# Kernel optimization log

Hardware: AMD Instinct MI355X
Metric: run time of the kernel (lower is better)

## Reference

```python
import jax, jax.numpy as jnp
import numpy as np

HEAD_DIM = 128
L2_EPS = 1e-6


def l2norm(x):
    # RMS-style L2Norm: computed in fp32, cast back (matches L2Norm.forward)
    x32 = x.astype(jnp.float32)
    y = x32 * jax.lax.rsqrt(jnp.mean(x32 * x32, axis=-1, keepdims=True) + L2_EPS)
    return y.astype(x.dtype)


def setup_inputs() -> dict:
    key = jax.random.key(0)
    ks = jax.random.split(key, 8)
    B, S, D = 16, 1, 4096
    NKV, HD, MAXS = 8, HEAD_DIM, 4096
    w_scale = 0.02
    return {
        "x": jax.random.normal(ks[0], (B, S, D), dtype=jnp.float32),
        "wq": jax.random.normal(ks[1], (D, D), dtype=jnp.float32) * w_scale,
        "wk": jax.random.normal(ks[2], (D, NKV * HD), dtype=jnp.float32) * w_scale,
        "wv": jax.random.normal(ks[3], (D, NKV * HD), dtype=jnp.float32) * w_scale,
        "wo": jax.random.normal(ks[4], (D, D), dtype=jnp.float32) * w_scale,
        "cache_k": jax.random.normal(ks[5], (B, MAXS, NKV, HD), dtype=jnp.float32),
        "cache_v": jax.random.normal(ks[6], (B, MAXS, NKV, HD), dtype=jnp.float32),
        "freqs_complex": jax.random.normal(ks[7], (1, 64), dtype=jnp.float32),  # unused, as in source
        "start_pos": 4095,
    }


def reference(x, wq, wk, wv, wo, cache_k, cache_v, freqs_complex, start_pos):
    b, s, d = x.shape
    hd = HEAD_DIM
    n_kv = cache_k.shape[2]
    n_q = wq.shape[1] // hd
    n_rep = n_q // n_kv

    # QKV projections (Linear, no bias)
    xq = (x @ wq).reshape(b, s, n_q, hd)
    xk = (x @ wk).reshape(b, s, n_kv, hd)
    xv = (x @ wv).reshape(b, s, n_kv, hd)

    # qk_norm active since dim <= 4096
    xq = l2norm(xq)
    xk = l2norm(xk)

    # KV-cache append at start_pos (start_pos is a static Python int)
    cache_k = jax.lax.dynamic_update_slice(cache_k, xk, (0, start_pos, 0, 0))
    cache_v = jax.lax.dynamic_update_slice(cache_v, xv, (0, start_pos, 0, 0))
    keys = cache_k[:, : start_pos + s]    # [b, T, n_kv, hd]
    values = cache_v[:, : start_pos + s]  # [b, T, n_kv, hd]

    # GQA: group query heads as (n_kv, n_rep); equivalent to repeat_kv without
    # materializing the repeated KV tensors.
    xq = xq.reshape(b, s, n_kv, n_rep, hd)
    scores = jnp.einsum("bqgrd,bkgd->bgrqk", xq, keys) / np.float32(np.sqrt(hd))
    scores = jax.nn.softmax(scores.astype(jnp.float32), axis=-1).astype(xq.dtype)
    out = jnp.einsum("bgrqk,bkgd->bqgrd", scores, values).reshape(b, s, n_q * hd)
    return out @ wo
```

## Files before the change

### kernel.cpp

```cpp
#include <hip/hip_runtime.h>

#define D_MODEL 4096
#define NKV     8
#define NREP    4
#define HD      128
#define BATCH   16
#define SEQ     4096
#define NCOLS   6144
#define SPLITS  32
#define KC      128
#define NS      8
#define CHUNK   512

#define OFF_QKVP 0
#define OFF_QKV  3145728
#define OFF_ATTO 3244032
#define OFF_ATTM 3768320
#define OFF_ATTL 3772416
#define OFF_XO   3776512

__global__ __launch_bounds__(256) void qkv_partial(
    const float* __restrict__ x, const float* __restrict__ wq,
    const float* __restrict__ wk, const float* __restrict__ wv,
    float* __restrict__ part)
{
  int tid = threadIdx.x;
  int col = blockIdx.x * 256 + tid;
  int sp  = blockIdx.y;
  const float* w; int c; int N;
  if (col < 4096)      { w = wq; c = col;        N = 4096; }
  else if (col < 5120) { w = wk; c = col - 4096; N = 1024; }
  else                 { w = wv; c = col - 5120; N = 1024; }
  int k0 = sp * KC;
  const float* wp = w + (size_t)k0 * N + c;
  float acc[BATCH];
#pragma unroll
  for (int b = 0; b < BATCH; ++b) acc[b] = 0.f;
  for (int kk = 0; kk < KC; kk += 4) {
    float w0 = wp[0];
    float w1 = wp[N];
    float w2 = wp[2 * N];
    float w3 = wp[3 * N];
#pragma unroll
    for (int b = 0; b < BATCH; ++b) {
      float4 xb = *reinterpret_cast<const float4*>(x + b * D_MODEL + k0 + kk);
      acc[b] = fmaf(xb.x, w0, fmaf(xb.y, w1, fmaf(xb.z, w2, fmaf(xb.w, w3, acc[b]))));
    }
    wp += (size_t)4 * N;
  }
#pragma unroll
  for (int b = 0; b < BATCH; ++b)
    part[(size_t)(sp * BATCH + b) * NCOLS + col] = acc[b];
}

__global__ __launch_bounds__(128) void qkv_finalize(
    const float* __restrict__ part, float* __restrict__ qkv)
{
  __shared__ float red[2];
  int blk = blockIdx.x;
  int b = blk / 48, h = blk - b * 48;
  int col = h * HD + threadIdx.x;
  float v = 0.f;
#pragma unroll
  for (int s = 0; s < SPLITS; ++s)
    v += part[(size_t)(s * BATCH + b) * NCOLS + col];
  float ss = v * v;
#pragma unroll
  for (int off = 32; off; off >>= 1) ss += __shfl_xor(ss, off);
  if ((threadIdx.x & 63) == 0) red[threadIdx.x >> 6] = ss;
  __syncthreads();
  float tot = red[0] + red[1];
  if (h < 40)
    v *= rsqrtf(tot * (1.f / 128.f) + 1e-6f);
  qkv[(size_t)b * NCOLS + col] = v;
}

__global__ __launch_bounds__(256) void attn_partial(
    const float* __restrict__ cache_k, const float* __restrict__ cache_v,
    const float* __restrict__ qkv,
    float* __restrict__ attO, float* __restrict__ attM, float* __restrict__ attL)
{
  __shared__ float qs[NREP * HD];
  __shared__ float sc[NREP * CHUNK];
  __shared__ float op[4 * NREP * HD];
  __shared__ float ml[8];
  int tid = threadIdx.x;
  int sp = blockIdx.x;
  int bg = blockIdx.y;
  int b = bg >> 3, g = bg & 7;

  const float* qsrc = qkv + (size_t)b * NCOLS + g * (NREP * HD);
  for (int i = tid; i < NREP * HD; i += 256) qs[i] = qsrc[i];
  __syncthreads();

  int pos0 = sp * CHUNK;
  const float* kbase = cache_k + ((size_t)b * SEQ * NKV + g) * HD;
#pragma unroll
  for (int t = 0; t < 2; ++t) {
    int pos = pos0 + t * 256 + tid;
    const float* kv = (pos == SEQ - 1)
        ? (qkv + (size_t)b * NCOLS + 4096 + g * HD)
        : (kbase + (size_t)pos * (NKV * HD));
    float a0 = 0.f, a1 = 0.f, a2 = 0.f, a3 = 0.f;
    for (int d = 0; d < HD; d += 4) {
      float4 kk = *reinterpret_cast<const float4*>(kv + d);
      float4 q0 = *reinterpret_cast<const float4*>(qs + 0 * HD + d);
      float4 q1 = *reinterpret_cast<const float4*>(qs + 1 * HD + d);
      float4 q2 = *reinterpret_cast<const float4*>(qs + 2 * HD + d);
      float4 q3 = *reinterpret_cast<const float4*>(qs + 3 * HD + d);
      a0 += kk.x*q0.x + kk.y*q0.y + kk.z*q0.z + kk.w*q0.w;
      a1 += kk.x*q1.x + kk.y*q1.y + kk.z*q1.z + kk.w*q1.w;
      a2 += kk.x*q2.x + kk.y*q2.y + kk.z*q2.z + kk.w*q2.w;
      a3 += kk.x*q3.x + kk.y*q3.y + kk.z*q3.z + kk.w*q3.w;
    }
    const float scl = 0.08838834764831845f;
    sc[0 * CHUNK + t * 256 + tid] = a0 * scl;
    sc[1 * CHUNK + t * 256 + tid] = a1 * scl;
    sc[2 * CHUNK + t * 256 + tid] = a2 * scl;
    sc[3 * CHUNK + t * 256 + tid] = a3 * scl;
  }
  __syncthreads();

  int wv_ = tid >> 6, lane = tid & 63;
  {
    float vals[8];
    float m = -1e30f;
#pragma unroll
    for (int i = 0; i < 8; ++i) { vals[i] = sc[wv_ * CHUNK + i * 64 + lane]; m = fmaxf(m, vals[i]); }
#pragma unroll
    for (int off = 32; off; off >>= 1) m = fmaxf(m, __shfl_xor(m, off));
    float l = 0.f;
#pragma unroll
    for (int i = 0; i < 8; ++i) { float p = __expf(vals[i] - m); sc[wv_ * CHUNK + i * 64 + lane] = p; l += p; }
#pragma unroll
    for (int off = 32; off; off >>= 1) l += __shfl_xor(l, off);
    if (lane == 0) { ml[wv_] = m; ml[4 + wv_] = l; }
  }
  __syncthreads();

  int quarter = tid >> 6;
  int dl = (tid & 63) * 2;
  float a00=0,a01=0,a10=0,a11=0,a20=0,a21=0,a30=0,a31=0;
  const float* vbase = cache_v + ((size_t)b * SEQ * NKV + g) * HD;
  int pb = pos0 + quarter * 128;
  for (int j = 0; j < 128; ++j) {
    int pos = pb + j;
    const float* vvp = (pos == SEQ - 1)
        ? (qkv + (size_t)b * NCOLS + 5120 + g * HD)
        : (vbase + (size_t)pos * (NKV * HD));
    float2 vd = *reinterpret_cast<const float2*>(vvp + dl);
    float p0 = sc[0 * CHUNK + quarter * 128 + j];
    float p1 = sc[1 * CHUNK + quarter * 128 + j];
    float p2 = sc[2 * CHUNK + quarter * 128 + j];
    float p3 = sc[3 * CHUNK + quarter * 128 + j];
    a00 = fmaf(p0, vd.x, a00); a01 = fmaf(p0, vd.y, a01);
    a10 = fmaf(p1, vd.x, a10); a11 = fmaf(p1, vd.y, a11);
    a20 = fmaf(p2, vd.x, a20); a21 = fmaf(p2, vd.y, a21);
    a30 = fmaf(p3, vd.x, a30); a31 = fmaf(p3, vd.y, a31);
  }
  *reinterpret_cast<float2*>(op + (quarter * NREP + 0) * HD + dl) = make_float2(a00, a01);
  *reinterpret_cast<float2*>(op + (quarter * NREP + 1) * HD + dl) = make_float2(a10, a11);
  *reinterpret_cast<float2*>(op + (quarter * NREP + 2) * HD + dl) = make_float2(a20, a21);
  *reinterpret_cast<float2*>(op + (quarter * NREP + 3) * HD + dl) = make_float2(a30, a31);
  __syncthreads();

  size_t base = (size_t)(bg * NS + sp);
  for (int i = tid; i < NREP * HD; i += 256) {
    int r = i >> 7, d = i & 127;
    float o = op[(0*NREP + r)*HD + d] + op[(1*NREP + r)*HD + d]
            + op[(2*NREP + r)*HD + d] + op[(3*NREP + r)*HD + d];
    attO[base * (NREP * HD) + i] = o;
  }
  if (tid < 4)      attM[base * 4 + tid] = ml[tid];
  else if (tid < 8) attL[base * 4 + (tid - 4)] = ml[tid];
}

__global__ __launch_bounds__(512) void attn_combine(
    const float* __restrict__ attO, const float* __restrict__ attM,
    const float* __restrict__ attL, float* __restrict__ xo)
{
  int bg = blockIdx.x;
  int tid = threadIdx.x;
  int r = tid >> 7;
  float m_s[NS];
  float M = -1e30f;
#pragma unroll
  for (int s = 0; s < NS; ++s) {
    m_s[s] = attM[(size_t)(bg * NS + s) * 4 + r];
    M = fmaxf(M, m_s[s]);
  }
  float L = 0.f, o = 0.f;
#pragma unroll
  for (int s = 0; s < NS; ++s) {
    float f = __expf(m_s[s] - M);
    L += attL[(size_t)(bg * NS + s) * 4 + r] * f;
    o += attO[(size_t)(bg * NS + s) * 512 + tid] * f;
  }
  int b = bg >> 3, g = bg & 7;
  xo[(size_t)b * D_MODEL + g * 512 + tid] = o / L;
}

__global__ __launch_bounds__(256) void wo_partial(
    const float* __restrict__ xo, const float* __restrict__ wo,
    float* __restrict__ part)
{
  int tid = threadIdx.x;
  int col = blockIdx.x * 256 + tid;
  int sp  = blockIdx.y;
  int k0 = sp * KC;
  const float* wp = wo + (size_t)k0 * D_MODEL + col;
  float acc[BATCH];
#pragma unroll
  for (int b = 0; b < BATCH; ++b) acc[b] = 0.f;
  for (int kk = 0; kk < KC; kk += 4) {
    float w0 = wp[0];
    float w1 = wp[D_MODEL];
    float w2 = wp[2 * D_MODEL];
    float w3 = wp[3 * D_MODEL];
#pragma unroll
    for (int b = 0; b < BATCH; ++b) {
      float4 xb = *reinterpret_cast<const float4*>(xo + b * D_MODEL + k0 + kk);
      acc[b] = fmaf(xb.x, w0, fmaf(xb.y, w1, fmaf(xb.z, w2, fmaf(xb.w, w3, acc[b]))));
    }
    wp += (size_t)4 * D_MODEL;
  }
#pragma unroll
  for (int b = 0; b < BATCH; ++b)
    part[(size_t)(sp * BATCH + b) * D_MODEL + col] = acc[b];
}

__global__ __launch_bounds__(256) void wo_finalize(
    const float* __restrict__ part, float* __restrict__ out)
{
  int i = blockIdx.x * 256 + threadIdx.x;
  float v = 0.f;
#pragma unroll
  for (int s = 0; s < SPLITS; ++s)
    v += part[(size_t)s * (BATCH * D_MODEL) + i];
  out[i] = v;
}

extern "C" void kernel_launch(void* const* d_in, const int* in_sizes, int n_in,
                              void* d_out, int out_size, void* d_ws, size_t ws_size,
                              hipStream_t stream) {
  const float* x       = (const float*)d_in[0];
  const float* wq      = (const float*)d_in[1];
  const float* wk      = (const float*)d_in[2];
  const float* wv      = (const float*)d_in[3];
  const float* wo      = (const float*)d_in[4];
  const float* cache_k = (const float*)d_in[5];
  const float* cache_v = (const float*)d_in[6];
  float* out  = (float*)d_out;
  float* wsf  = (float*)d_ws;
  float* qkvp = wsf + OFF_QKVP;
  float* qkv  = wsf + OFF_QKV;
  float* attO = wsf + OFF_ATTO;
  float* attM = wsf + OFF_ATTM;
  float* attL = wsf + OFF_ATTL;
  float* xo   = wsf + OFF_XO;
  float* wop  = wsf + OFF_QKVP;

  qkv_partial <<<dim3(24, 32), 256, 0, stream>>>(x, wq, wk, wv, qkvp);
  qkv_finalize<<<BATCH * 48, 128, 0, stream>>>(qkvp, qkv);
  attn_partial<<<dim3(NS, BATCH * NKV), 256, 0, stream>>>(cache_k, cache_v, qkv, attO, attM, attL);
  attn_combine<<<BATCH * NKV, 512, 0, stream>>>(attO, attM, attL, xo);
  wo_partial  <<<dim3(16, 32), 256, 0, stream>>>(xo, wo, wop);
  wo_finalize <<<256, 256, 0, stream>>>(wop, out);
}
```

Measured before the change: 692.9 us.

## Double attention splits, restructure PV loop per head, unroll GEMV k-loop

The attention split kernel now uses 16 splits of 256 positions instead of 8 of 512, which doubles the number of blocks. The grid is reordered so the batch-group index is on x, and the kernel gets a launch-bounds occupancy hint. The PV stage now gives each wave one query head over the whole chunk, writing directly to global memory. This removes the shared-memory cross-quarter reduction and two syncs, but all four waves now read the same V rows. The QKV and Wo GEMV k-loops load 8 weight rows per step with unroll 2 for more memory-level parallelism, and workspace buffers are aliased to shrink the layout.

Result: slower. 740.5 us (+6.9%).

```diff
diff --git a/kernel.cpp b/kernel.cpp
--- a/kernel.cpp
+++ b/kernel.cpp
@@ -9,15 +9,16 @@
 #define NCOLS   6144
 #define SPLITS  32
 #define KC      128
-#define NS      8
-#define CHUNK   512
+#define NS      16
+#define CHUNK   256
 
 #define OFF_QKVP 0
+#define OFF_ATTO 0
+#define OFF_WOP  0
 #define OFF_QKV  3145728
-#define OFF_ATTO 3244032
-#define OFF_ATTM 3768320
-#define OFF_ATTL 3772416
-#define OFF_XO   3776512
+#define OFF_ATTM 3244032
+#define OFF_ATTL 3252224
+#define OFF_XO   3260416
 
 __global__ __launch_bounds__(256) void qkv_partial(
     const float* __restrict__ x, const float* __restrict__ wq,
@@ -36,17 +37,23 @@
   float acc[BATCH];
 #pragma unroll
   for (int b = 0; b < BATCH; ++b) acc[b] = 0.f;
-  for (int kk = 0; kk < KC; kk += 4) {
-    float w0 = wp[0];
-    float w1 = wp[N];
-    float w2 = wp[2 * N];
-    float w3 = wp[3 * N];
+#pragma unroll 2
+  for (int kk = 0; kk < KC; kk += 8) {
+    float wr[8];
+#pragma unroll
+    for (int j = 0; j < 8; ++j) wr[j] = wp[(size_t)j * N];
 #pragma unroll
     for (int b = 0; b < BATCH; ++b) {
-      float4 xb = *reinterpret_cast<const float4*>(x + b * D_MODEL + k0 + kk);
-      acc[b] = fmaf(xb.x, w0, fmaf(xb.y, w1, fmaf(xb.z, w2, fmaf(xb.w, w3, acc[b]))));
-    }
-    wp += (size_t)4 * N;
+      float4 xa = *reinterpret_cast<const float4*>(x + b * D_MODEL + k0 + kk);
+      float4 xb = *reinterpret_cast<const float4*>(x + b * D_MODEL + k0 + kk + 4);
+      float t = acc[b];
+      t = fmaf(xa.x, wr[0], t); t = fmaf(xa.y, wr[1], t);
+      t = fmaf(xa.z, wr[2], t); t = fmaf(xa.w, wr[3], t);
+      t = fmaf(xb.x, wr[4], t); t = fmaf(xb.y, wr[5], t);
+      t = fmaf(xb.z, wr[6], t); t = fmaf(xb.w, wr[7], t);
+      acc[b] = t;
+    }
+    wp += (size_t)8 * N;
   }
 #pragma unroll
   for (int b = 0; b < BATCH; ++b)
@@ -75,18 +82,16 @@
   qkv[(size_t)b * NCOLS + col] = v;
 }
 
-__global__ __launch_bounds__(256) void attn_partial(
+__global__ __launch_bounds__(256, 4) void attn_partial(
     const float* __restrict__ cache_k, const float* __restrict__ cache_v,
     const float* __restrict__ qkv,
     float* __restrict__ attO, float* __restrict__ attM, float* __restrict__ attL)
 {
   __shared__ float qs[NREP * HD];
   __shared__ float sc[NREP * CHUNK];
-  __shared__ float op[4 * NREP * HD];
-  __shared__ float ml[8];
-  int tid = threadIdx.x;
-  int sp = blockIdx.x;
-  int bg = blockIdx.y;
+  int tid = threadIdx.x;
+  int bg = blockIdx.x;
+  int sp = blockIdx.y;
   int b = bg >> 3, g = bg & 7;
 
   const float* qsrc = qkv + (size_t)b * NCOLS + g * (NREP * HD);
@@ -94,85 +99,77 @@
   __syncthreads();
 
   int pos0 = sp * CHUNK;
-  const float* kbase = cache_k + ((size_t)b * SEQ * NKV + g) * HD;
-#pragma unroll
-  for (int t = 0; t < 2; ++t) {
-    int pos = pos0 + t * 256 + tid;
+
+  {
+    int pos = pos0 + tid;
     const float* kv = (pos == SEQ - 1)
         ? (qkv + (size_t)b * NCOLS + 4096 + g * HD)
-        : (kbase + (size_t)pos * (NKV * HD));
-    float a0 = 0.f, a1 = 0.f, a2 = 0.f, a3 = 0.f;
-    for (int d = 0; d < HD; d += 4) {
-      float4 kk = *reinterpret_cast<const float4*>(kv + d);
-      float4 q0 = *reinterpret_cast<const float4*>(qs + 0 * HD + d);
-      float4 q1 = *reinterpret_cast<const float4*>(qs + 1 * HD + d);
-      float4 q2 = *reinterpret_cast<const float4*>(qs + 2 * HD + d);
-      float4 q3 = *reinterpret_cast<const float4*>(qs + 3 * HD + d);
-      a0 += kk.x*q0.x + kk.y*q0.y + kk.z*q0.z + kk.w*q0.w;
-      a1 += kk.x*q1.x + kk.y*q1.y + kk.z*q1.z + kk.w*q1.w;
-      a2 += kk.x*q2.x + kk.y*q2.y + kk.z*q2.z + kk.w*q2.w;
-      a3 += kk.x*q3.x + kk.y*q3.y + kk.z*q3.z + kk.w*q3.w;
+        : (cache_k + ((size_t)b * SEQ * NKV + g) * HD + (size_t)pos * (NKV * HD));
+    float a[NREP];
+#pragma unroll
+    for (int r = 0; r < NREP; ++r) a[r] = 0.f;
+#pragma unroll
+    for (int c = 0; c < 4; ++c) {
+      float4 kr[8];
+#pragma unroll
+      for (int j = 0; j < 8; ++j)
+        kr[j] = *reinterpret_cast<const float4*>(kv + c * 32 + j * 4);
+#pragma unroll
+      for (int r = 0; r < NREP; ++r) {
+        float s = 0.f;
+#pragma unroll
+        for (int j = 0; j < 8; ++j) {
+          float4 qv = *reinterpret_cast<const float4*>(qs + r * HD + c * 32 + j * 4);
+          s += kr[j].x * qv.x + kr[j].y * qv.y + kr[j].z * qv.z + kr[j].w * qv.w;
+        }
+        a[r] += s;
+      }
     }
     const float scl = 0.08838834764831845f;
-    sc[0 * CHUNK + t * 256 + tid] = a0 * scl;
-    sc[1 * CHUNK + t * 256 + tid] = a1 * scl;
-    sc[2 * CHUNK + t * 256 + tid] = a2 * scl;
-    sc[3 * CHUNK + t * 256 + tid] = a3 * scl;
+#pragma unroll
+    for (int r = 0; r < NREP; ++r) sc[r * CHUNK + tid] = a[r] * scl;
   }
   __syncthreads();
 
   int wv_ = tid >> 6, lane = tid & 63;
+  float m_reg, l_reg;
   {
-    float vals[8];
+    float vals[4];
     float m = -1e30f;
 #pragma unroll
-    for (int i = 0; i < 8; ++i) { vals[i] = sc[wv_ * CHUNK + i * 64 + lane]; m = fmaxf(m, vals[i]); }
+    for (int i = 0; i < 4; ++i) { vals[i] = sc[wv_ * CHUNK + i * 64 + lane]; m = fmaxf(m, vals[i]); }
 #pragma unroll
     for (int off = 32; off; off >>= 1) m = fmaxf(m, __shfl_xor(m, off));
     float l = 0.f;
 #pragma unroll
-    for (int i = 0; i < 8; ++i) { float p = __expf(vals[i] - m); sc[wv_ * CHUNK + i * 64 + lane] = p; l += p; }
+    for (int i = 0; i < 4; ++i) { float p = __expf(vals[i] - m); sc[wv_ * CHUNK + i * 64 + lane] = p; l += p; }
 #pragma unroll
     for (int off = 32; off; off >>= 1) l += __shfl_xor(l, off);
-    if (lane == 0) { ml[wv_] = m; ml[4 + wv_] = l; }
-  }
-  __syncthreads();
-
-  int quarter = tid >> 6;
-  int dl = (tid & 63) * 2;
-  float a00=0,a01=0,a10=0,a11=0,a20=0,a21=0,a30=0,a31=0;
-  const float* vbase = cache_v + ((size_t)b * SEQ * NKV + g) * HD;
-  int pb = pos0 + quarter * 128;
-  for (int j = 0; j < 128; ++j) {
-    int pos = pb + j;
-    const float* vvp = (pos == SEQ - 1)
-        ? (qkv + (size_t)b * NCOLS + 5120 + g * HD)
-        : (vbase + (size_t)pos * (NKV * HD));
-    float2 vd = *reinterpret_cast<const float2*>(vvp + dl);
-    float p0 = sc[0 * CHUNK + quarter * 128 + j];
-    float p1 = sc[1 * CHUNK + quarter * 128 + j];
-    float p2 = sc[2 * CHUNK + quarter * 128 + j];
-    float p3 = sc[3 * CHUNK + quarter * 128 + j];
-    a00 = fmaf(p0, vd.x, a00); a01 = fmaf(p0, vd.y, a01);
-    a10 = fmaf(p1, vd.x, a10); a11 = fmaf(p1, vd.y, a11);
-    a20 = fmaf(p2, vd.x, a20); a21 = fmaf(p2, vd.y, a21);
-    a30 = fmaf(p3, vd.x, a30); a31 = fmaf(p3, vd.y, a31);
-  }
-  *reinterpret_cast<float2*>(op + (quarter * NREP + 0) * HD + dl) = make_float2(a00, a01);
-  *reinterpret_cast<float2*>(op + (quarter * NREP + 1) * HD + dl) = make_float2(a10, a11);
-  *reinterpret_cast<float2*>(op + (quarter * NREP + 2) * HD + dl) = make_float2(a20, a21);
-  *reinterpret_cast<float2*>(op + (quarter * NREP + 3) * HD + dl) = make_float2(a30, a31);
-  __syncthreads();
-
-  size_t base = (size_t)(bg * NS + sp);
-  for (int i = tid; i < NREP * HD; i += 256) {
-    int r = i >> 7, d = i & 127;
-    float o = op[(0*NREP + r)*HD + d] + op[(1*NREP + r)*HD + d]
-            + op[(2*NREP + r)*HD + d] + op[(3*NREP + r)*HD + d];
-    attO[base * (NREP * HD) + i] = o;
-  }
-  if (tid < 4)      attM[base * 4 + tid] = ml[tid];
-  else if (tid < 8) attL[base * 4 + (tid - 4)] = ml[tid];
+    m_reg = m; l_reg = l;
+  }
+  __syncthreads();
+
+  {
+    int dl = lane * 2;
+    const float* vbase  = cache_v + ((size_t)b * SEQ * NKV + g) * HD;
+    const float* vfresh = qkv + (size_t)b * NCOLS + 5120 + g * HD;
+    const float* pr = sc + wv_ * CHUNK;
+    float ax = 0.f, ay = 0.f;
+    for (int j = 0; j < CHUNK; j += 8) {
+#pragma unroll
+      for (int u = 0; u < 8; ++u) {
+        int pos = pos0 + j + u;
+        const float* vp = (pos == SEQ - 1) ? vfresh : (vbase + (size_t)pos * (NKV * HD));
+        float2 vd = *reinterpret_cast<const float2*>(vp + dl);
+        float p = pr[j + u];
+        ax = fmaf(p, vd.x, ax);
+        ay = fmaf(p, vd.y, ay);
+      }
+    }
+    size_t base = (size_t)(bg * NS + sp);
+    *reinterpret_cast<float2*>(attO + base * (NREP * HD) + wv_ * HD + dl) = make_float2(ax, ay);
+    if (lane == 0) { attM[base * 4 + wv_] = m_reg; attL[base * 4 + wv_] = l_reg; }
+  }
 }
 
 __global__ __launch_bounds__(512) void attn_combine(
@@ -212,17 +209,23 @@
   float acc[BATCH];
 #pragma unroll
   for (int b = 0; b < BATCH; ++b) acc[b] = 0.f;
-  for (int kk = 0; kk < KC; kk += 4) {
-    float w0 = wp[0];
-    float w1 = wp[D_MODEL];
-    float w2 = wp[2 * D_MODEL];
-    float w3 = wp[3 * D_MODEL];
+#pragma unroll 2
+  for (int kk = 0; kk < KC; kk += 8) {
+    float wr[8];
+#pragma unroll
+    for (int j = 0; j < 8; ++j) wr[j] = wp[(size_t)j * D_MODEL];
 #pragma unroll
     for (int b = 0; b < BATCH; ++b) {
-      float4 xb = *reinterpret_cast<const float4*>(xo + b * D_MODEL + k0 + kk);
-      acc[b] = fmaf(xb.x, w0, fmaf(xb.y, w1, fmaf(xb.z, w2, fmaf(xb.w, w3, acc[b]))));
-    }
-    wp += (size_t)4 * D_MODEL;
+      float4 xa = *reinterpret_cast<const float4*>(xo + b * D_MODEL + k0 + kk);
+      float4 xb = *reinterpret_cast<const float4*>(xo + b * D_MODEL + k0 + kk + 4);
+      float t = acc[b];
+      t = fmaf(xa.x, wr[0], t); t = fmaf(xa.y, wr[1], t);
+      t = fmaf(xa.z, wr[2], t); t = fmaf(xa.w, wr[3], t);
+      t = fmaf(xb.x, wr[4], t); t = fmaf(xb.y, wr[5], t);
+      t = fmaf(xb.z, wr[6], t); t = fmaf(xb.w, wr[7], t);
+      acc[b] = t;
+    }
+    wp += (size_t)8 * D_MODEL;
   }
 #pragma unroll
   for (int b = 0; b < BATCH; ++b)
@@ -258,11 +261,11 @@
   float* attM = wsf + OFF_ATTM;
   float* attL = wsf + OFF_ATTL;
   float* xo   = wsf + OFF_XO;
-  float* wop  = wsf + OFF_QKVP;
+  float* wop  = wsf + OFF_WOP;
 
   qkv_partial <<<dim3(24, 32), 256, 0, stream>>>(x, wq, wk, wv, qkvp);
   qkv_finalize<<<BATCH * 48, 128, 0, stream>>>(qkvp, qkv);
-  attn_partial<<<dim3(NS, BATCH * NKV), 256, 0, stream>>>(cache_k, cache_v, qkv, attO, attM, attL);
+  attn_partial<<<dim3(BATCH * NKV, NS), 256, 0, stream>>>(cache_k, cache_v, qkv, attO, attM, attL);
   attn_combine<<<BATCH * NKV, 512, 0, stream>>>(attO, attM, attL, xo);
   wo_partial  <<<dim3(16, 32), 256, 0, stream>>>(xo, wo, wop);
   wo_finalize <<<256, 256, 0, stream>>>(wop, out);
```
